# Performance work log

Measured on AMD Instinct MI355X. Metric: run time of the kernel, lower is better.

The kernel has to match this reference:

```python
import jax, jax.numpy as jnp
import numpy as np

NUM_HEADS = 4
WINDOW = 3

def setup_inputs() -> dict:
    key = jax.random.key(0)
    ks = jax.random.split(key, 6)
    B, V, C, H, W = 4, 6, 256, 32, 32
    s = 0.02
    return {
        "x": jax.random.normal(ks[0], (B, V, C, H, W), jnp.float32),
        "Wq": jax.random.normal(ks[1], (C, C), jnp.float32) * s,
        "bq": jnp.zeros((C,), jnp.float32),
        "Wk": jax.random.normal(ks[2], (V * C, C), jnp.float32) * s,
        "bk": jnp.zeros((C,), jnp.float32),
        "Wv": jax.random.normal(ks[3], (V * C, C), jnp.float32) * s,
        "bv": jnp.zeros((C,), jnp.float32),
        "Wo": jax.random.normal(ks[4], (C, C), jnp.float32) * s,
        "bo": jnp.zeros((C,), jnp.float32),
    }

def reference(x, Wq, bq, Wk, bk, Wv, bv, Wo, bo):
    B, V, C, H, W = x.shape
    HW = H * W
    S = HW * V  # query sequence length
    nh = NUM_HEADS
    hd = C // nh
    # q: [B, V, H, W, C] -> [B, S, C]
    q_in = jnp.transpose(x, (0, 1, 3, 4, 2)).reshape(B, S, C)
    # k/v input: [B, H, W, V, C] -> [B, HW, V*C]
    kv_in = jnp.transpose(x, (0, 3, 4, 1, 2)).reshape(B, HW, V * C)
    q = q_in @ Wq + bq
    k = kv_in @ Wk + bk
    v = kv_in @ Wv + bv
    q = q.reshape(B, S, nh, hd).transpose(0, 2, 1, 3)    # [B, nh, S, hd]
    k = k.reshape(B, HW, nh, hd).transpose(0, 2, 1, 3)   # [B, nh, HW, hd]
    v = v.reshape(B, HW, nh, hd).transpose(0, 2, 1, 3)   # [B, nh, HW, hd]
    logits = jnp.einsum("bhqd,bhkd->bhqk", q, k) / jnp.sqrt(jnp.float32(hd))
    # Faithful mask: row i has ones in columns [max(0,i-W), i+W] (clipped to HW cols);
    # it is ADDED as mask * -1e9, masking OUT the diagonal window (as in source).
    i = jnp.arange(S)[:, None]
    j = jnp.arange(HW)[None, :]
    mask = ((j >= i - WINDOW) & (j < i + WINDOW + 1)).astype(logits.dtype)
    logits = logits + mask * (-1e9)
    attn = jax.nn.softmax(logits, axis=-1)
    out = jnp.einsum("bhqk,bhkd->bhqd", attn, v)         # [B, nh, S, hd]
    out = out.transpose(0, 2, 1, 3).reshape(B, S, C)
    out = out @ Wo + bo
    return x.reshape(B * V, C, H, W) + out.reshape(B * V, C, H, W)
```

## Files before the change

### kernel.cpp

```cpp
#include <hip/hip_runtime.h>
#include <cstddef>

namespace {

constexpr int B=4, V=6, C=256, HWS=1024, S=6144, NH=4, HD=64, VC=1536;

typedef short short8  __attribute__((ext_vector_type(8)));
typedef short short4v __attribute__((ext_vector_type(4)));
typedef float f32x4   __attribute__((ext_vector_type(4)));

__device__ inline short f2bf(float f){
  union{float f; unsigned u;} v; v.f=f;
  unsigned r = v.u + 0x7fffu + ((v.u>>16)&1u);
  return (short)(r>>16);
}
__device__ inline unsigned fbits(float f){
  union{float f; unsigned u;} v; v.f=f; return v.u;
}

typedef const __attribute__((address_space(1))) unsigned* gas_t;
typedef __attribute__((address_space(3))) unsigned* las_t;
__device__ inline void gll(const void* g, void* l){
  __builtin_amdgcn_global_load_lds((gas_t)g, (las_t)l, 16, 0, 0);
}

__device__ inline void tr_tile(const float* in, int inRow, short* out, int outRow,
                               int r0, int c0, int t){
  const int tx=t&15, ty=t>>4;
  float a[4][4];
  #pragma unroll
  for(int i=0;i<4;i++){
    const float4 f=*(const float4*)(in + (size_t)(r0+ty*4+i)*inRow + c0 + tx*4);
    a[i][0]=f.x; a[i][1]=f.y; a[i][2]=f.z; a[i][3]=f.w;
  }
  #pragma unroll
  for(int j=0;j<4;j++){
    short4v o4;
    #pragma unroll
    for(int i=0;i<4;i++) o4[i]=f2bf(a[i][j]);
    *(short4v*)(out + (size_t)(c0+tx*4+j)*outRow + r0+ty*4) = o4;
  }
}

__global__ __launch_bounds__(256) void prep(const float* __restrict__ x,
                                            const float* __restrict__ Wq, const float* __restrict__ Wk,
                                            const float* __restrict__ Wv, const float* __restrict__ Wo,
                                            short* __restrict__ xb, short* __restrict__ WqT,
                                            short* __restrict__ WkT, short* __restrict__ WvT,
                                            short* __restrict__ WoT){
  const int blk=blockIdx.x;
  if(blk<1536){
    const int bx=blk&15, by=(blk>>4)&3, bv=blk>>6;
    tr_tile(x + (size_t)bv*C*HWS, HWS, xb + (size_t)bv*HWS*C, C, by*64, bx*64, threadIdx.x);
  } else {
    const int idx=blk-1536;
    const int tile=idx%96, z=idx/96;
    const float* in; short* out; int R;
    if(z==0){in=Wq; out=WqT; R=C;}
    else if(z==1){in=Wo; out=WoT; R=C;}
    else if(z==2){in=Wk; out=WkT; R=VC;}
    else         {in=Wv; out=WvT; R=VC;}
    const int tilesC=C/64, ntiles=(R/64)*tilesC;
    if(tile>=ntiles) return;
    tr_tile(in, C, out, R, (tile/tilesC)*64, (tile%tilesC)*64, threadIdx.x);
  }
}

template<int MODE>
__device__ inline void qo_body(const short* __restrict__ A, const short* __restrict__ BT,
                               const float* __restrict__ bias, const float* __restrict__ xres,
                               void* __restrict__ outv, short* sh, int n0, int r0){
  const int t=threadIdx.x, lane=t&63, w=t>>6, quad=lane>>4, ln=lane&15;
  f32x4 acc[2][4];
  #pragma unroll
  for(int rt=0;rt<2;rt++)
    #pragma unroll
    for(int nt=0;nt<4;nt++) acc[rt][nt]=(f32x4)0.f;

  const int sr=w*8+(lane>>3), scc=(lane&7)*8;
  auto stage=[&](int it,int bufi){
    const int k0=it*64;
    short* dst = sh + bufi*12288;
    const short* Asrc = A + (size_t)r0*C + k0;
    #pragma unroll
    for(int cc=0; cc<4; cc++)
      gll(Asrc + (size_t)(sr+cc*32)*C + scc, dst + cc*2048 + w*512);
    const short* Bsrc = BT + (size_t)n0*C + k0;
    gll(Bsrc + (size_t)sr*C + scc,      dst + 8192 + w*512);
    gll(Bsrc + (size_t)(sr+32)*C + scc, dst + 8192 + 2048 + w*512);
  };

  stage(0,0);
  __syncthreads();
  for(int it=0; it<4; it++){
    if(it<3) stage(it+1,(it+1)&1);
    const short* As_=sh+(it&1)*12288;
    const short* Bs_=As_+8192;
    #pragma unroll
    for(int s=0;s<2;s++){
      const short8 af0=*(const short8*)&As_[(w*32+ln)*64    + s*32+quad*8];
      const short8 af1=*(const short8*)&As_[(w*32+16+ln)*64 + s*32+quad*8];
      #pragma unroll
      for(int nt=0;nt<4;nt++){
        const short8 bf=*(const short8*)&Bs_[(nt*16+ln)*64 + s*32+quad*8];
        acc[0][nt]=__builtin_amdgcn_mfma_f32_16x16x32_bf16(af0,bf,acc[0][nt],0,0,0);
        acc[1][nt]=__builtin_amdgcn_mfma_f32_16x16x32_bf16(af1,bf,acc[1][nt],0,0,0);
      }
    }
    __syncthreads();
  }

  constexpr float QSCALE = 0.18033688011112042f;
  float bcol[4];
  #pragma unroll
  for(int nt=0;nt<4;nt++) bcol[nt]=bias[n0+nt*16+ln];
  #pragma unroll
  for(int rt=0;rt<2;rt++)
    #pragma unroll
    for(int nt=0;nt<4;nt++)
      #pragma unroll
      for(int i=0;i<4;i++){
        const int row=r0+w*32+rt*16+quad*4+i, col=n0+nt*16+ln;
        const float vv=acc[rt][nt][i]+bcol[nt];
        if constexpr(MODE==0) ((short*)outv)[(size_t)row*C+col]=f2bf(vv*QSCALE);
        else ((float*)outv)[(size_t)row*C+col]=vv + xres[(size_t)row*C+col];
      }
}

__global__ __launch_bounds__(256) void proj(const short* __restrict__ xb,
                                            const short* __restrict__ WqT, const short* __restrict__ WkT,
                                            const short* __restrict__ WvT,
                                            const float* __restrict__ bq, const float* __restrict__ bk,
                                            const float* __restrict__ bv,
                                            short* __restrict__ qb, short* __restrict__ Kpack,
                                            short* __restrict__ Vpack){
  __shared__ __align__(16) short sh[24576];
  const int blk=blockIdx.x;
  const int t=threadIdx.x, lane=t&63, w=t>>6, quad=lane>>4, ln=lane&15;

  if(blk>=256){
    const int qblk=blk-256;
    qo_body<0>(xb, WqT, bq, nullptr, qb, sh, (qblk&3)*64, (qblk>>2)*128);
    return;
  }

  const int n0=(blk&3)*64, r0=(blk>>2)*64;
  const int b=r0>>10, hw0=r0&1023;
  const int h=n0>>6, bh=b*NH+h;

  f32x4 ak[4], av[4];
  #pragma unroll
  for(int nt=0;nt<4;nt++){ ak[nt]=(f32x4)0.f; av[nt]=(f32x4)0.f; }

  const int sr=w*8+(lane>>3), scc=(lane&7)*8;
  auto stageKV=[&](int it,int bufi){
    const int k0=it*64, v=k0>>8, c0=k0&255;
    short* dst = sh + bufi*12288;
    const short* As_src = xb + (size_t)((b*V+v)*HWS + hw0)*C + c0;
    gll(As_src + (size_t)sr*C + scc,       dst + w*512);
    gll(As_src + (size_t)(sr+32)*C + scc,  dst + 2048 + w*512);
    const short* Bk_src = WkT + (size_t)n0*VC + k0;
    gll(Bk_src + (size_t)sr*VC + scc,      dst + 4096 + w*512);
    gll(Bk_src + (size_t)(sr+32)*VC + scc, dst + 4096 + 2048 + w*512);
    const short* Bv_src = WvT + (size_t)n0*VC + k0;
    gll(Bv_src + (size_t)sr*VC + scc,      dst + 8192 + w*512);
    gll(Bv_src + (size_t)(sr+32)*VC + scc, dst + 8192 + 2048 + w*512);
  };

  stageKV(0,0);
  __syncthreads();
  for(int it=0; it<24; it++){
    if(it<23) stageKV(it+1,(it+1)&1);
    const short* As_=sh+(it&1)*12288;
    const short* Bk_=As_+4096;
    const short* Bv_=As_+8192;
    #pragma unroll
    for(int s=0;s<2;s++){
      const short8 af=*(const short8*)&As_[(w*16+ln)*64 + s*32+quad*8];
      #pragma unroll
      for(int nt=0;nt<4;nt++){
        const short8 kf=*(const short8*)&Bk_[(nt*16+ln)*64 + s*32+quad*8];
        const short8 vf=*(const short8*)&Bv_[(nt*16+ln)*64 + s*32+quad*8];
        ak[nt]=__builtin_amdgcn_mfma_f32_16x16x32_bf16(af,kf,ak[nt],0,0,0);
        av[nt]=__builtin_amdgcn_mfma_f32_16x16x32_bf16(af,vf,av[nt],0,0,0);
      }
    }
    __syncthreads();
  }

  float bkc[4], bvc[4];
  #pragma unroll
  for(int nt=0;nt<4;nt++){ bkc[nt]=bk[n0+nt*16+ln]; bvc[nt]=bv[n0+nt*16+ln]; }

  {
    short* vq = Vpack + ((size_t)(bh*64 + (hw0>>4) + w))*1024;
    #pragma unroll
    for(int nt=0;nt<4;nt++){
      short4v vp;
      #pragma unroll
      for(int i=0;i<4;i++) vp[i]=f2bf(av[nt][i]+bvc[nt]);
      *(short4v*)(vq + nt*256 + lane*4) = vp;
    }
  }

  __syncthreads();
  #pragma unroll
  for(int nt=0;nt<4;nt++)
    #pragma unroll
    for(int i=0;i<4;i++)
      sh[(w*16+quad*4+i)*72 + nt*16+ln] = f2bf(ak[nt][i]+bkc[nt]);
  __syncthreads();
  {
    short* kp = Kpack + ((size_t)(bh*64 + (hw0>>4) + w))*1024;
    #pragma unroll
    for(int half=0; half<2; half++){
      const short8 f = *(short8*)&sh[(w*16+ln)*72 + half*32 + quad*8];
      *(short8*)(kp + half*512 + lane*8) = f;
    }
  }
}

__global__ __launch_bounds__(512,4) void attn_k(const short* __restrict__ q, const short* __restrict__ Kpack,
                                                const short* __restrict__ Vpack, short* __restrict__ ao){
  __shared__ __align__(16) char smem[50176];
  short* KV   = (short*)smem;
  float* obuf = (float*)smem;
  float* lbuf = (float*)(smem + 49152);

  const int blk=blockIdx.x;
  const int bh=(blk&7)*2 + ((blk>>3)&1);
  const int qt=blk>>4;
  const int b=bh>>2, h=bh&3;
  const int s0=qt*128;
  const int t=threadIdx.x, lane=t&63, w=t>>6, quad=lane>>4, ln=lane&15;
  const int wq=w&3, wk=w>>2;

  short8 qf[2][2];
  #pragma unroll
  for(int ntl=0;ntl<2;ntl++)
    #pragma unroll
    for(int s=0;s<2;s++)
      qf[ntl][s]=*(const short8*)&q[(size_t)(b*S+s0+wq*32+ntl*16+ln)*C + h*HD + s*32+quad*8];

  f32x4 o[4][2];
  #pragma unroll
  for(int dt=0;dt<4;dt++)
    #pragma unroll
    for(int ntl=0;ntl<2;ntl++) o[dt][ntl]=(f32x4)0.f;
  f32x4 l4[2];
  l4[0]=(f32x4)0.f; l4[1]=(f32x4)0.f;

  const short* Kt = Kpack + (size_t)bh*65536;
  const short* Vt = Vpack + (size_t)bh*65536;
  const f32x4 z4=(f32x4)0.f;
  const int rb = s0 + wq*32;

  gll(Kt + w*512 + lane*8,        KV + w*512);
  gll(Vt + w*512 + lane*8,        KV + 4096 + w*512);
  gll(Kt + 4096 + w*512 + lane*8, KV + 8192 + w*512);
  gll(Vt + 4096 + w*512 + lane*8, KV + 8192 + 4096 + w*512);

  int cb = 0;
  int pb = 2;
  #pragma unroll 1
  for(int TI=0; TI<16; TI++){
    if(TI<15) asm volatile("s_waitcnt vmcnt(2) lgkmcnt(0)\n\ts_barrier" ::: "memory");
    else      asm volatile("s_waitcnt vmcnt(0) lgkmcnt(0)\n\ts_barrier" ::: "memory");

    if(TI<14){
      gll(Kt + (size_t)(TI+2)*4096 + w*512 + lane*8, KV + pb*8192 + w*512);
      gll(Vt + (size_t)(TI+2)*4096 + w*512 + lane*8, KV + pb*8192 + 4096 + w*512);
    }

    const short* Kb = KV + cb*8192;
    const short* Vb = Kb + 4096;

    const short8 kf00=*(const short8*)&Kb[wk*2048 + lane*8];
    const short8 kf01=*(const short8*)&Kb[wk*2048 + 512 + lane*8];
    const short8 kf10=*(const short8*)&Kb[wk*2048 + 1024 + lane*8];
    const short8 kf11=*(const short8*)&Kb[wk*2048 + 1536 + lane*8];

    f32x4 sa[2][2];
    __builtin_amdgcn_s_setprio(1);
    #pragma unroll
    for(int ntl=0;ntl<2;ntl++){
      sa[0][ntl]=__builtin_amdgcn_mfma_f32_16x16x32_bf16(kf00,qf[ntl][0],z4,0,0,0);
      sa[0][ntl]=__builtin_amdgcn_mfma_f32_16x16x32_bf16(kf01,qf[ntl][1],sa[0][ntl],0,0,0);
      sa[1][ntl]=__builtin_amdgcn_mfma_f32_16x16x32_bf16(kf10,qf[ntl][0],z4,0,0,0);
      sa[1][ntl]=__builtin_amdgcn_mfma_f32_16x16x32_bf16(kf11,qf[ntl][1],sa[1][ntl],0,0,0);
    }
    __builtin_amdgcn_s_setprio(0);

    short4v vf[2][4];
    #pragma unroll
    for(int kt=0;kt<2;kt++)
      #pragma unroll
      for(int dt=0;dt<4;dt++)
        vf[kt][dt]=*(const short4v*)&Vb[wk*2048 + kt*1024 + dt*256 + lane*4];

    const int kmin=TI*64 + wk*32;
    if(kmin+31 >= rb-3 && kmin <= rb+34){
      #pragma unroll
      for(int kt=0;kt<2;kt++)
        #pragma unroll
        for(int ntl=0;ntl<2;ntl++){
          const int ig=rb+ntl*16+ln;
          #pragma unroll
          for(int i=0;i<4;i++){
            const int jg=kmin+kt*16+quad*4+i;
            if((unsigned)(jg-ig+3)<=6u) sa[kt][ntl][i]=-100.f;
          }
        }
    }

    short4v pt[2][2];
    #pragma unroll
    for(int kt=0;kt<2;kt++)
      #pragma unroll
      for(int ntl=0;ntl<2;ntl++){
        f32x4 pv;
        #pragma unroll
        for(int i=0;i<4;i++) pv[i]=__builtin_amdgcn_exp2f(sa[kt][ntl][i]);
        l4[ntl]+=pv;
        union{ short4v s; unsigned u[2]; } P;
        P.u[0]=__builtin_amdgcn_perm(fbits(pv[1]), fbits(pv[0]), 0x07060302u);
        P.u[1]=__builtin_amdgcn_perm(fbits(pv[3]), fbits(pv[2]), 0x07060302u);
        pt[kt][ntl]=P.s;
      }

    __builtin_amdgcn_s_setprio(1);
    #pragma unroll
    for(int kt=0;kt<2;kt++)
      #pragma unroll
      for(int dt=0;dt<4;dt++)
        #pragma unroll
        for(int ntl=0;ntl<2;ntl++)
          o[dt][ntl]=__builtin_amdgcn_mfma_f32_16x16x16bf16_1k(vf[kt][dt],pt[kt][ntl],o[dt][ntl],0,0,0);
    __builtin_amdgcn_s_setprio(0);

    cb = (cb==2)?0:cb+1;
    pb = (pb==2)?0:pb+1;
  }

  __syncthreads();

  float l[2];
  #pragma unroll
  for(int ntl=0;ntl<2;ntl++){
    l[ntl]=l4[ntl][0]+l4[ntl][1]+l4[ntl][2]+l4[ntl][3];
    l[ntl]+=__shfl_xor(l[ntl],16);
    l[ntl]+=__shfl_xor(l[ntl],32);
  }
  if(quad==0){
    lbuf[w*32+ln]    = l[0];
    lbuf[w*32+16+ln] = l[1];
  }
  if(wk==0){
    #pragma unroll
    for(int dt=0;dt<4;dt++)
      #pragma unroll
      for(int ntl=0;ntl<2;ntl++)
        #pragma unroll
        for(int i=0;i<4;i++)
          obuf[(dt*16+quad*4+i)*132 + wq*32+ntl*16+ln] = o[dt][ntl][i];
  }
  __syncthreads();
  if(wk==1){
    #pragma unroll
    for(int dt=0;dt<4;dt++)
      #pragma unroll
      for(int ntl=0;ntl<2;ntl++)
        #pragma unroll
        for(int i=0;i<4;i++)
          obuf[(dt*16+quad*4+i)*132 + wq*32+ntl*16+ln] += o[dt][ntl][i];
  }
  __syncthreads();

  {
    const int row=t>>2, dg=t&3;
    const float linv=1.0f/(lbuf[(row>>5)*32 + (row&31)] + lbuf[(4+(row>>5))*32 + (row&31)]);
    short tmp[16];
    #pragma unroll
    for(int j=0;j<16;j++) tmp[j]=f2bf(obuf[(dg*16+j)*132+row]*linv);
    short* op = ao + (size_t)(b*S+s0+row)*C + h*HD + dg*16;
    *(short8*)op     = *(short8*)&tmp[0];
    *(short8*)(op+8) = *(short8*)&tmp[8];
  }
}

__global__ __launch_bounds__(256) void o_gemm(const short* __restrict__ A, const short* __restrict__ BT,
                                              const float* __restrict__ bias, const float* __restrict__ xres,
                                              float* __restrict__ out){
  __shared__ __align__(16) short sh[24576];
  qo_body<1>(A, BT, bias, xres, out, sh, (int)(blockIdx.x&3)*64, (int)(blockIdx.x>>2)*128);
}

}

extern "C" void kernel_launch(void* const* d_in, const int* in_sizes, int n_in,
                              void* d_out, int out_size, void* d_ws, size_t ws_size,
                              hipStream_t stream) {
  const float* x  = (const float*)d_in[0];
  const float* Wq = (const float*)d_in[1];
  const float* bq = (const float*)d_in[2];
  const float* Wk = (const float*)d_in[3];
  const float* bk = (const float*)d_in[4];
  const float* Wv = (const float*)d_in[5];
  const float* bv = (const float*)d_in[6];
  const float* Wo = (const float*)d_in[7];
  const float* bo = (const float*)d_in[8];
  float* out = (float*)d_out;

  char* p = (char*)d_ws;
  const size_t szBS=(size_t)B*S*C*2, szK=(size_t)B*HWS*C*2;
  short* xb   =(short*)p; p+=szBS;
  short* qb   =(short*)p; p+=szBS;
  short* aob  =(short*)p; p+=szBS;
  short* Kpack=(short*)p; p+=szK;
  short* Vpack=(short*)p; p+=szK;
  short* WqT=(short*)p; p+=(size_t)C*C*2;
  short* WoT=(short*)p; p+=(size_t)C*C*2;
  short* WkT=(short*)p; p+=(size_t)C*VC*2;
  short* WvT=(short*)p; p+=(size_t)C*VC*2;

  prep<<<dim3(1920), 256, 0, stream>>>(x, Wq,Wk,Wv,Wo, xb, WqT,WkT,WvT,WoT);
  proj<<<dim3(1024), 256, 0, stream>>>(xb, WqT,WkT,WvT, bq,bk,bv, qb, Kpack, Vpack);
  attn_k<<<dim3(B*NH*(S/128)), 512, 0, stream>>>(qb, Kpack, Vpack, aob);
  o_gemm<<<dim3(4*((B*S)/128)), 256, 0, stream>>>(aob, WoT, bo, x, out);
}
```

Before: 167.3 us.

## Give each attention wave all keys for 32 queries, removing cross-wave reduction

The attention kernel changes from 8 waves (4 query groups × 2 key halves) per 128-query tile to 6 waves per 192-query tile. Each wave now walks both key halves of every staged K/V chunk itself. This removes the LDS round-trip and extra barriers that summed partial outputs and row sums across waves, and each K/V tile is reused by more queries. The cost is more serial MFMA work per wave, fewer blocks (384 instead of 768), and an uneven split of async loads across waves, which needs per-wave vmcnt waits.

```diff
diff --git a/kernel.cpp b/kernel.cpp
--- a/kernel.cpp
+++ b/kernel.cpp
@@ -220,27 +220,24 @@
   }
 }
 
-__global__ __launch_bounds__(512,4) void attn_k(const short* __restrict__ q, const short* __restrict__ Kpack,
+__global__ __launch_bounds__(384,3) void attn_k(const short* __restrict__ q, const short* __restrict__ Kpack,
                                                 const short* __restrict__ Vpack, short* __restrict__ ao){
-  __shared__ __align__(16) char smem[50176];
-  short* KV   = (short*)smem;
-  float* obuf = (float*)smem;
-  float* lbuf = (float*)(smem + 49152);
+  __shared__ __align__(16) char smem[49152];
+  short* KV = (short*)smem;
 
   const int blk=blockIdx.x;
   const int bh=(blk&7)*2 + ((blk>>3)&1);
   const int qt=blk>>4;
   const int b=bh>>2, h=bh&3;
-  const int s0=qt*128;
+  const int s0=qt*192;
   const int t=threadIdx.x, lane=t&63, w=t>>6, quad=lane>>4, ln=lane&15;
-  const int wq=w&3, wk=w>>2;
 
   short8 qf[2][2];
   #pragma unroll
   for(int ntl=0;ntl<2;ntl++)
     #pragma unroll
     for(int s=0;s<2;s++)
-      qf[ntl][s]=*(const short8*)&q[(size_t)(b*S+s0+wq*32+ntl*16+ln)*C + h*HD + s*32+quad*8];
+      qf[ntl][s]=*(const short8*)&q[(size_t)(b*S+s0+w*32+ntl*16+ln)*C + h*HD + s*32+quad*8];
 
   f32x4 o[4][2];
   #pragma unroll
@@ -253,138 +250,130 @@
   const short* Kt = Kpack + (size_t)bh*65536;
   const short* Vt = Vpack + (size_t)bh*65536;
   const f32x4 z4=(f32x4)0.f;
-  const int rb = s0 + wq*32;
-
-  gll(Kt + w*512 + lane*8,        KV + w*512);
-  gll(Vt + w*512 + lane*8,        KV + 4096 + w*512);
-  gll(Kt + 4096 + w*512 + lane*8, KV + 8192 + w*512);
-  gll(Vt + 4096 + w*512 + lane*8, KV + 8192 + 4096 + w*512);
-
-  int cb = 0;
-  int pb = 2;
+  const int rb = s0 + w*32;
+
+  auto stage=[&](int TI,int bufi){
+    short* db = KV + bufi*8192;
+    for(int c=w; c<16; c+=6){
+      const short* src = (c<8?Kt:Vt) + (size_t)TI*4096 + (size_t)(c&7)*512 + lane*8;
+      gll(src, db + c*512);
+    }
+  };
+  stage(0,0);
+  stage(1,1);
+
+  int cb=0, pb=2;
   #pragma unroll 1
   for(int TI=0; TI<16; TI++){
-    if(TI<15) asm volatile("s_waitcnt vmcnt(2) lgkmcnt(0)\n\ts_barrier" ::: "memory");
-    else      asm volatile("s_waitcnt vmcnt(0) lgkmcnt(0)\n\ts_barrier" ::: "memory");
-
-    if(TI<14){
-      gll(Kt + (size_t)(TI+2)*4096 + w*512 + lane*8, KV + pb*8192 + w*512);
-      gll(Vt + (size_t)(TI+2)*4096 + w*512 + lane*8, KV + pb*8192 + 4096 + w*512);
-    }
+    if(TI<15){
+      if(w<4) asm volatile("s_waitcnt vmcnt(3) lgkmcnt(0)" ::: "memory");
+      else    asm volatile("s_waitcnt vmcnt(2) lgkmcnt(0)" ::: "memory");
+    } else {
+      asm volatile("s_waitcnt vmcnt(0) lgkmcnt(0)" ::: "memory");
+    }
+    asm volatile("s_barrier" ::: "memory");
+
+    if(TI<14) stage(TI+2, pb);
 
     const short* Kb = KV + cb*8192;
     const short* Vb = Kb + 4096;
 
-    const short8 kf00=*(const short8*)&Kb[wk*2048 + lane*8];
-    const short8 kf01=*(const short8*)&Kb[wk*2048 + 512 + lane*8];
-    const short8 kf10=*(const short8*)&Kb[wk*2048 + 1024 + lane*8];
-    const short8 kf11=*(const short8*)&Kb[wk*2048 + 1536 + lane*8];
-
-    f32x4 sa[2][2];
-    __builtin_amdgcn_s_setprio(1);
-    #pragma unroll
-    for(int ntl=0;ntl<2;ntl++){
-      sa[0][ntl]=__builtin_amdgcn_mfma_f32_16x16x32_bf16(kf00,qf[ntl][0],z4,0,0,0);
-      sa[0][ntl]=__builtin_amdgcn_mfma_f32_16x16x32_bf16(kf01,qf[ntl][1],sa[0][ntl],0,0,0);
-      sa[1][ntl]=__builtin_amdgcn_mfma_f32_16x16x32_bf16(kf10,qf[ntl][0],z4,0,0,0);
-      sa[1][ntl]=__builtin_amdgcn_mfma_f32_16x16x32_bf16(kf11,qf[ntl][1],sa[1][ntl],0,0,0);
-    }
-    __builtin_amdgcn_s_setprio(0);
-
-    short4v vf[2][4];
-    #pragma unroll
-    for(int kt=0;kt<2;kt++)
-      #pragma unroll
-      for(int dt=0;dt<4;dt++)
-        vf[kt][dt]=*(const short4v*)&Vb[wk*2048 + kt*1024 + dt*256 + lane*4];
-
-    const int kmin=TI*64 + wk*32;
-    if(kmin+31 >= rb-3 && kmin <= rb+34){
+    #pragma unroll 1
+    for(int kh=0; kh<2; kh++){
+      const short8 kf00=*(const short8*)&Kb[kh*2048 + lane*8];
+      const short8 kf01=*(const short8*)&Kb[kh*2048 + 512 + lane*8];
+      const short8 kf10=*(const short8*)&Kb[kh*2048 + 1024 + lane*8];
+      const short8 kf11=*(const short8*)&Kb[kh*2048 + 1536 + lane*8];
+
+      f32x4 sa[2][2];
+      __builtin_amdgcn_s_setprio(1);
+      #pragma unroll
+      for(int ntl=0;ntl<2;ntl++){
+        sa[0][ntl]=__builtin_amdgcn_mfma_f32_16x16x32_bf16(kf00,qf[ntl][0],z4,0,0,0);
+        sa[0][ntl]=__builtin_amdgcn_mfma_f32_16x16x32_bf16(kf01,qf[ntl][1],sa[0][ntl],0,0,0);
+        sa[1][ntl]=__builtin_amdgcn_mfma_f32_16x16x32_bf16(kf10,qf[ntl][0],z4,0,0,0);
+        sa[1][ntl]=__builtin_amdgcn_mfma_f32_16x16x32_bf16(kf11,qf[ntl][1],sa[1][ntl],0,0,0);
+      }
+      __builtin_amdgcn_s_setprio(0);
+
+      short4v vf[2][4];
+      #pragma unroll
+      for(int kt=0;kt<2;kt++)
+        #pragma unroll
+        for(int dt=0;dt<4;dt++)
+          vf[kt][dt]=*(const short4v*)&Vb[kh*2048 + kt*1024 + dt*256 + lane*4];
+
+      const int kmin=TI*64 + kh*32;
+      if(kmin+31 >= rb-3 && kmin <= rb+34){
+        #pragma unroll
+        for(int kt=0;kt<2;kt++)
+          #pragma unroll
+          for(int ntl=0;ntl<2;ntl++){
+            const int ig=rb+ntl*16+ln;
+            #pragma unroll
+            for(int i=0;i<4;i++){
+              const int jg=kmin+kt*16+quad*4+i;
+              if((unsigned)(jg-ig+3)<=6u) sa[kt][ntl][i]=-100.f;
+            }
+          }
+      }
+
+      short4v pt[2][2];
       #pragma unroll
       for(int kt=0;kt<2;kt++)
         #pragma unroll
         for(int ntl=0;ntl<2;ntl++){
-          const int ig=rb+ntl*16+ln;
+          f32x4 pv;
           #pragma unroll
-          for(int i=0;i<4;i++){
-            const int jg=kmin+kt*16+quad*4+i;
-            if((unsigned)(jg-ig+3)<=6u) sa[kt][ntl][i]=-100.f;
-          }
+          for(int i=0;i<4;i++) pv[i]=__builtin_amdgcn_exp2f(sa[kt][ntl][i]);
+          l4[ntl]+=pv;
+          union{ short4v s; unsigned u[2]; } P;
+          P.u[0]=__builtin_amdgcn_perm(fbits(pv[1]), fbits(pv[0]), 0x07060302u);
+          P.u[1]=__builtin_amdgcn_perm(fbits(pv[3]), fbits(pv[2]), 0x07060302u);
+          pt[kt][ntl]=P.s;
         }
-    }
-
-    short4v pt[2][2];
-    #pragma unroll
-    for(int kt=0;kt<2;kt++)
-      #pragma unroll
-      for(int ntl=0;ntl<2;ntl++){
-        f32x4 pv;
+
+      __builtin_amdgcn_s_setprio(1);
+      #pragma unroll
+      for(int kt=0;kt<2;kt++)
         #pragma unroll
-        for(int i=0;i<4;i++) pv[i]=__builtin_amdgcn_exp2f(sa[kt][ntl][i]);
-        l4[ntl]+=pv;
-        union{ short4v s; unsigned u[2]; } P;
-        P.u[0]=__builtin_amdgcn_perm(fbits(pv[1]), fbits(pv[0]), 0x07060302u);
-        P.u[1]=__builtin_amdgcn_perm(fbits(pv[3]), fbits(pv[2]), 0x07060302u);
-        pt[kt][ntl]=P.s;
-      }
-
-    __builtin_amdgcn_s_setprio(1);
-    #pragma unroll
-    for(int kt=0;kt<2;kt++)
-      #pragma unroll
-      for(int dt=0;dt<4;dt++)
-        #pragma unroll
-        for(int ntl=0;ntl<2;ntl++)
-          o[dt][ntl]=__builtin_amdgcn_mfma_f32_16x16x16bf16_1k(vf[kt][dt],pt[kt][ntl],o[dt][ntl],0,0,0);
-    __builtin_amdgcn_s_setprio(0);
+        for(int dt=0;dt<4;dt++)
+          #pragma unroll
+          for(int ntl=0;ntl<2;ntl++)
+            o[dt][ntl]=__builtin_amdgcn_mfma_f32_16x16x16bf16_1k(vf[kt][dt],pt[kt][ntl],o[dt][ntl],0,0,0);
+      __builtin_amdgcn_s_setprio(0);
+    }
 
     cb = (cb==2)?0:cb+1;
     pb = (pb==2)?0:pb+1;
   }
 
-  __syncthreads();
-
-  float l[2];
+  float linv[2];
   #pragma unroll
   for(int ntl=0;ntl<2;ntl++){
-    l[ntl]=l4[ntl][0]+l4[ntl][1]+l4[ntl][2]+l4[ntl][3];
-    l[ntl]+=__shfl_xor(l[ntl],16);
-    l[ntl]+=__shfl_xor(l[ntl],32);
-  }
-  if(quad==0){
-    lbuf[w*32+ln]    = l[0];
-    lbuf[w*32+16+ln] = l[1];
-  }
-  if(wk==0){
-    #pragma unroll
-    for(int dt=0;dt<4;dt++)
-      #pragma unroll
-      for(int ntl=0;ntl<2;ntl++)
-        #pragma unroll
-        for(int i=0;i<4;i++)
-          obuf[(dt*16+quad*4+i)*132 + wq*32+ntl*16+ln] = o[dt][ntl][i];
-  }
-  __syncthreads();
-  if(wk==1){
-    #pragma unroll
-    for(int dt=0;dt<4;dt++)
-      #pragma unroll
-      for(int ntl=0;ntl<2;ntl++)
-        #pragma unroll
-        for(int i=0;i<4;i++)
-          obuf[(dt*16+quad*4+i)*132 + wq*32+ntl*16+ln] += o[dt][ntl][i];
-  }
-  __syncthreads();
-
-  {
-    const int row=t>>2, dg=t&3;
-    const float linv=1.0f/(lbuf[(row>>5)*32 + (row&31)] + lbuf[(4+(row>>5))*32 + (row&31)]);
-    short tmp[16];
-    #pragma unroll
-    for(int j=0;j<16;j++) tmp[j]=f2bf(obuf[(dg*16+j)*132+row]*linv);
-    short* op = ao + (size_t)(b*S+s0+row)*C + h*HD + dg*16;
-    *(short8*)op     = *(short8*)&tmp[0];
-    *(short8*)(op+8) = *(short8*)&tmp[8];
+    float l=l4[ntl][0]+l4[ntl][1]+l4[ntl][2]+l4[ntl][3];
+    l+=__shfl_xor(l,16);
+    l+=__shfl_xor(l,32);
+    linv[ntl]=1.0f/l;
+  }
+
+  __syncthreads();
+
+  #pragma unroll
+  for(int dt=0;dt<4;dt++)
+    #pragma unroll
+    for(int ntl=0;ntl<2;ntl++){
+      short4v ob;
+      #pragma unroll
+      for(int i=0;i<4;i++) ob[i]=f2bf(o[dt][ntl][i]*linv[ntl]);
+      *(short4v*)&KV[(size_t)(w*32+ntl*16+ln)*80 + dt*16+quad*4] = ob;
+    }
+  __syncthreads();
+
+  #pragma unroll
+  for(int k=0;k<4;k++){
+    const int id=t+k*384, r=id>>3, c=id&7;
+    *(short8*)(ao + (size_t)(b*S+s0+r)*C + h*HD + c*8) = *(const short8*)&KV[(size_t)r*80 + c*8];
   }
 }
 
@@ -425,6 +414,6 @@
 
   prep<<<dim3(1920), 256, 0, stream>>>(x, Wq,Wk,Wv,Wo, xb, WqT,WkT,WvT,WoT);
   proj<<<dim3(1024), 256, 0, stream>>>(xb, WqT,WkT,WvT, bq,bk,bv, qb, Kpack, Vpack);
-  attn_k<<<dim3(B*NH*(S/128)), 512, 0, stream>>>(qb, Kpack, Vpack, aob);
+  attn_k<<<dim3(B*NH*(S/192)), 384, 0, stream>>>(qb, Kpack, Vpack, aob);
   o_gemm<<<dim3(4*((B*S)/128)), 256, 0, stream>>>(aob, WoT, bo, x, out);
 }
```

New measurement: 178.9 us. +6.9%, slower.
